# Optimization experiments

Hardware: AMD Instinct MI355X
Metric: run time of the kernel (lower is better)

Reference implementation:

```python
import math
import jax, jax.numpy as jnp
import numpy as np

N, L, C, H, E = 50000, 3, 64, 4, 800000
D = C // H


def setup_inputs() -> dict:
    key = jax.random.key(0)
    ks = jax.random.split(key, 10)
    s = 1.0 / math.sqrt(C)
    return {
        "history": jax.random.normal(ks[0], (N, L, C), dtype=jnp.float32),
        "edge_index": jax.random.randint(ks[1], (2, E), 0, N, dtype=jnp.int32),
        "Wq": jax.random.normal(ks[2], (C, C), dtype=jnp.float32) * s,
        "bq": jnp.zeros((C,), dtype=jnp.float32),
        "Wk": jax.random.normal(ks[3], (C, C), dtype=jnp.float32) * s,
        "bk": jnp.zeros((C,), dtype=jnp.float32),
        "Wv": jax.random.normal(ks[4], (C, C), dtype=jnp.float32) * s,
        "bv": jnp.zeros((C,), dtype=jnp.float32),
        "Wo": jax.random.normal(ks[5], (C, C), dtype=jnp.float32) * s,
        "bo": jnp.zeros((C,), dtype=jnp.float32),
    }


def reference(history, edge_index, Wq, bq, Wk, bk, Wv, bv, Wo, bo):
    row, col = edge_index[0], edge_index[1]
    current = history[:, -1]                                   # [N, C]
    # torch Linear: y = x @ W.T + b
    q = (current @ Wq.T + bq).reshape(N, H, D)                  # [N, H, D]
    k = (history @ Wk.T + bk).reshape(N, L, H, D)               # [N, L, H, D]
    v = (history @ Wv.T + bv).reshape(N, L, H, D)

    q_dst = q[col][:, None]                                     # [E, 1, H, D]
    k_src = k[row]                                              # [E, L, H, D]
    scores = (q_dst * k_src).sum(-1) / math.sqrt(D)             # [E, L, H]
    token_w = jax.nn.softmax(scores, axis=1)                    # layer attention
    edge_msg = (token_w[..., None] * v[row]).sum(axis=1)        # [E, H, D]

    # edge_softmax over incoming edges of each destination node (per head)
    edge_scores = scores.max(axis=1)                            # [E, H]
    seg_max = jax.ops.segment_max(edge_scores, col, num_segments=N)
    seg_max = jnp.where(jnp.isfinite(seg_max), seg_max, 0.0)
    e = jnp.exp(edge_scores - seg_max[col])                     # [E, H]
    denom = jax.ops.segment_sum(e, col, num_segments=N)         # [N, H]
    edge_w = e / denom[col]                                     # [E, H]

    out = jnp.zeros((N, H, D), dtype=current.dtype)
    out = out.at[col].add(edge_msg * edge_w[..., None])          # scatter-add
    out = out.reshape(N, C)
    return out @ Wo.T + bo + current
```

## Files before the change

kernel.cpp:

```cpp
#include <hip/hip_runtime.h>

#define DEV __device__ __forceinline__

constexpr int L = 3;
constexpr int C = 64;
constexpr int H = 4;
constexpr int CAP = 64;

typedef unsigned short ushort8v __attribute__((ext_vector_type(8)));
typedef unsigned short ushort4v __attribute__((ext_vector_type(4)));
typedef short short8v __attribute__((ext_vector_type(8)));
typedef float f32x4 __attribute__((ext_vector_type(4)));

DEV float4 ld4g(const float* p) { return *reinterpret_cast<const float4*>(p); }
DEV void st4g(float* p, float4 v) { *reinterpret_cast<float4*>(p) = v; }
DEV float b2f(unsigned short u) {
    union { float f; unsigned int i; } x; x.i = ((unsigned int)u) << 16; return x.f;
}
DEV unsigned short f2b(float f) {
    unsigned int u = __float_as_uint(f);
    return (unsigned short)((u + 0x7FFFu + ((u >> 16) & 1u)) >> 16);
}
DEV float dot8(float4 a, float4 b, ushort8v k) {
    return a.x*b2f(k[0]) + a.y*b2f(k[1]) + a.z*b2f(k[2]) + a.w*b2f(k[3])
         + b.x*b2f(k[4]) + b.y*b2f(k[5]) + b.z*b2f(k[6]) + b.w*b2f(k[7]);
}
DEV void acc8(float4& A, float4& B, float w, ushort8v v) {
    A.x = fmaf(w, b2f(v[0]), A.x); A.y = fmaf(w, b2f(v[1]), A.y);
    A.z = fmaf(w, b2f(v[2]), A.z); A.w = fmaf(w, b2f(v[3]), A.w);
    B.x = fmaf(w, b2f(v[4]), B.x); B.y = fmaf(w, b2f(v[5]), B.y);
    B.z = fmaf(w, b2f(v[6]), B.z); B.w = fmaf(w, b2f(v[7]), B.w);
}

__global__ __launch_bounds__(256) void qkv_kernel(
    const float* __restrict__ history,
    const float* __restrict__ Wk, const float* __restrict__ bk,
    const float* __restrict__ Wv, const float* __restrict__ bv,
    const float* __restrict__ Wq, const float* __restrict__ bq,
    unsigned short* __restrict__ kvout, float* __restrict__ qout,
    const int* __restrict__ ei, int* __restrict__ counts, int* __restrict__ srcs,
    int N, int E, int nkvBlocks)
{
    __shared__ __align__(16) unsigned short WL[2][4096];
    __shared__ __align__(16) unsigned short ST[4][2048];

    {
        int gid = blockIdx.x * 256 + threadIdx.x;
        if (gid < E) {
            int c = ei[E + gid];
            int r = atomicAdd(&counts[c], 1);
            if (r < CAP) srcs[c * CAP + r] = ei[gid];
        }
    }

    const bool isKV = (int)blockIdx.x < nkvBlocks;
    const int nqBlocks = (N + 63) / 64;
    if (!isKV && (int)blockIdx.x >= nkvBlocks + nqBlocks) return;
    const int rowBase = (isKV ? blockIdx.x : (blockIdx.x - nkvBlocks)) * 64;
    const int totalRows = isKV ? N * L : N;
    const int tid = threadIdx.x;

    {
        const float* W1 = isKV ? Wk : Wq;
        const int col = tid >> 2;
        const int kc = (tid & 3) << 4;
        #pragma unroll
        for (int g = 0; g < 2; ++g) {
            int k0 = kc + g * 8;
            float4 wa = ld4g(&W1[col * 64 + k0]);
            float4 wb = ld4g(&W1[col * 64 + k0 + 4]);
            ushort8v t;
            t[0] = f2b(wa.x); t[1] = f2b(wa.y); t[2] = f2b(wa.z); t[3] = f2b(wa.w);
            t[4] = f2b(wb.x); t[5] = f2b(wb.y); t[6] = f2b(wb.z); t[7] = f2b(wb.w);
            *(ushort8v*)&WL[0][(k0 >> 3) * 512 + col * 8] = t;
        }
        if (isKV) {
            #pragma unroll
            for (int g = 0; g < 2; ++g) {
                int k0 = kc + g * 8;
                float4 wa = ld4g(&Wv[col * 64 + k0]);
                float4 wb = ld4g(&Wv[col * 64 + k0 + 4]);
                ushort8v t;
                t[0] = f2b(wa.x); t[1] = f2b(wa.y); t[2] = f2b(wa.z); t[3] = f2b(wa.w);
                t[4] = f2b(wb.x); t[5] = f2b(wb.y); t[6] = f2b(wb.z); t[7] = f2b(wb.w);
                *(ushort8v*)&WL[1][(k0 >> 3) * 512 + col * 8] = t;
            }
        }
    }
    __syncthreads();

    const int lane = tid & 63;
    const int wid = tid >> 6;
    const int rbase = rowBase + wid * 16;
    const int kg = lane >> 4;
    const int kbase = kg << 3;
    const int bcol = lane & 15;

    const int arow = min(rbase + (lane & 15), totalRows - 1);
    const size_t srcRow = isKV ? (size_t)arow : ((size_t)arow * L + (L - 1));
    const float* xp = &history[srcRow * C];
    float4 xa = ld4g(xp + kbase), xb = ld4g(xp + kbase + 4);
    float4 xc = ld4g(xp + 32 + kbase), xd = ld4g(xp + 32 + kbase + 4);
    short8v a0, a1;
    a0[0] = (short)f2b(xa.x); a0[1] = (short)f2b(xa.y);
    a0[2] = (short)f2b(xa.z); a0[3] = (short)f2b(xa.w);
    a0[4] = (short)f2b(xb.x); a0[5] = (short)f2b(xb.y);
    a0[6] = (short)f2b(xb.z); a0[7] = (short)f2b(xb.w);
    a1[0] = (short)f2b(xc.x); a1[1] = (short)f2b(xc.y);
    a1[2] = (short)f2b(xc.z); a1[3] = (short)f2b(xc.w);
    a1[4] = (short)f2b(xd.x); a1[5] = (short)f2b(xd.y);
    a1[6] = (short)f2b(xd.z); a1[7] = (short)f2b(xd.w);

    const f32x4 zero = {0.f, 0.f, 0.f, 0.f};

    if (isKV) {
        f32x4 aK[4] = {zero, zero, zero, zero};
        f32x4 aV[4] = {zero, zero, zero, zero};
        #pragma unroll
        for (int ct = 0; ct < 4; ++ct) {
            int col = ct * 16 + bcol;
            short8v bk0 = *(const short8v*)&WL[0][(kg) * 512 + col * 8];
            short8v bk1 = *(const short8v*)&WL[0][(4 + kg) * 512 + col * 8];
            short8v bv0 = *(const short8v*)&WL[1][(kg) * 512 + col * 8];
            short8v bv1 = *(const short8v*)&WL[1][(4 + kg) * 512 + col * 8];
            aK[ct] = __builtin_amdgcn_mfma_f32_16x16x32_bf16(a0, bk0, aK[ct], 0, 0, 0);
            aK[ct] = __builtin_amdgcn_mfma_f32_16x16x32_bf16(a1, bk1, aK[ct], 0, 0, 0);
            aV[ct] = __builtin_amdgcn_mfma_f32_16x16x32_bf16(a0, bv0, aV[ct], 0, 0, 0);
            aV[ct] = __builtin_amdgcn_mfma_f32_16x16x32_bf16(a1, bv1, aV[ct], 0, 0, 0);
        }
        unsigned short* st = &ST[wid][0];
        #pragma unroll
        for (int ct = 0; ct < 4; ++ct) {
            int col = ct * 16 + bcol;
            float biasK = bk[col];
            float biasV = bv[col];
            #pragma unroll
            for (int i = 0; i < 4; ++i) {
                int r = kg * 4 + i;
                int ck = col, cv = 64 + col;
                int pk = r * 128 + ((((ck >> 3) ^ r) & 15) << 3) + (ck & 7);
                int pv = r * 128 + ((((cv >> 3) ^ r) & 15) << 3) + (cv & 7);
                st[pk] = f2b(aK[ct][i] + biasK);
                st[pv] = f2b(aV[ct][i] + biasV);
            }
        }
        asm volatile("s_waitcnt lgkmcnt(0)" ::: "memory");
        unsigned short* base = kvout + (size_t)rbase * 128;
        #pragma unroll
        for (int i = 0; i < 4; ++i) {
            int chunk = i * 64 + lane;
            int r = chunk >> 4;
            int cc = chunk & 15;
            if (rbase + r < totalRows) {
                ushort8v vls = *(const ushort8v*)&st[(r * 16 + ((cc ^ r) & 15)) * 8];
                *(ushort8v*)(base + chunk * 8) = vls;
            }
        }
    } else {
        f32x4 aQ[4] = {zero, zero, zero, zero};
        #pragma unroll
        for (int ct = 0; ct < 4; ++ct) {
            int col = ct * 16 + bcol;
            short8v bq0 = *(const short8v*)&WL[0][(kg) * 512 + col * 8];
            short8v bq1 = *(const short8v*)&WL[0][(4 + kg) * 512 + col * 8];
            aQ[ct] = __builtin_amdgcn_mfma_f32_16x16x32_bf16(a0, bq0, aQ[ct], 0, 0, 0);
            aQ[ct] = __builtin_amdgcn_mfma_f32_16x16x32_bf16(a1, bq1, aQ[ct], 0, 0, 0);
        }
        float* stf = (float*)&ST[wid][0];
        #pragma unroll
        for (int ct = 0; ct < 4; ++ct) {
            int col = ct * 16 + bcol;
            float bias = bq[col];
            #pragma unroll
            for (int i = 0; i < 4; ++i) {
                int r = kg * 4 + i;
                int p = r * 64 + ((((col >> 2) ^ r) & 15) << 2) + (col & 3);
                stf[p] = (aQ[ct][i] + bias) * 0.25f;
            }
        }
        asm volatile("s_waitcnt lgkmcnt(0)" ::: "memory");
        float* baseq = qout + (size_t)rbase * 64;
        #pragma unroll
        for (int i = 0; i < 4; ++i) {
            int chunk = i * 64 + lane;
            int r = chunk >> 4;
            int cc = chunk & 15;
            if (rbase + r < totalRows) {
                float4 vq = *(const float4*)&stf[(r * 16 + ((cc ^ r) & 15)) * 4];
                *(float4*)(baseq + chunk * 4) = vq;
            }
        }
    }
}

__global__ __launch_bounds__(256) void gather_kernel(
    const int* __restrict__ srcs, const int* __restrict__ counts,
    const float* __restrict__ q, const unsigned short* __restrict__ kv,
    const float* __restrict__ history,
    const float* __restrict__ Wo, const float* __restrict__ bo,
    float* __restrict__ out, int N)
{
    __shared__ __align__(16) unsigned short WoS[4096];
    __shared__ float boS[64];
    __shared__ float sc4[4][64];

    const int tid = threadIdx.x;
    #pragma unroll
    for (int j = 0; j < 16; ++j) {
        int idx = tid + (j << 8);
        int c = idx >> 6, i = idx & 63;
        int phys = (c << 6) | ((((i >> 2) ^ c) & 15) << 2) | (i & 3);
        WoS[phys] = f2b(Wo[idx]);
    }
    if (tid < 64) boS[tid] = bo[tid];
    __syncthreads();

    const int n = blockIdx.x * 4 + (tid >> 6);
    if (n >= N) return;
    const int lane = tid & 63;
    const int wid = tid >> 6;
    float* sc = &sc4[wid][0];

    const int sub = lane >> 3;
    const int ld = lane & 7;
    const int c0 = ld << 3;
    const int wrow = lane << 6;

    const int start = n * CAP;
    const int cnt = min(counts[n], CAP);

    const float xv = history[((size_t)n * L + (L - 1)) * C + lane];
    const float4 qa = ld4g(&q[(size_t)n * C + c0]);
    const float4 qb = ld4g(&q[(size_t)n * C + c0 + 4]);
    float4 ma = make_float4(0.f, 0.f, 0.f, 0.f);
    float4 mb = make_float4(0.f, 0.f, 0.f, 0.f);
    float dsum = 0.f;

    for (int i = sub; i < cnt; i += 8) {
        const int src = srcs[start + i];
        const unsigned short* kb = kv + (size_t)src * (L * 2 * C) + c0;
        ushort8v k0 = *(const ushort8v*)(kb);
        ushort8v k1 = *(const ushort8v*)(kb + 2 * C);
        ushort8v k2 = *(const ushort8v*)(kb + 4 * C);

        float s0 = dot8(qa, qb, k0);
        float s1 = dot8(qa, qb, k1);
        float s2 = dot8(qa, qb, k2);
        s0 += __shfl_xor(s0, 1);
        s1 += __shfl_xor(s1, 1);
        s2 += __shfl_xor(s2, 1);

        float e0 = __expf(s0), e1 = __expf(s1), e2 = __expf(s2);
        float ee = fmaxf(fmaxf(e0, e1), e2);
        float scl = ee / (e0 + e1 + e2);
        float w0 = e0 * scl, w1 = e1 * scl, w2 = e2 * scl;

        ushort8v v0 = *(const ushort8v*)(kb + C);
        ushort8v v1 = *(const ushort8v*)(kb + 3 * C);
        ushort8v v2 = *(const ushort8v*)(kb + 5 * C);
        acc8(ma, mb, w0, v0);
        acc8(ma, mb, w1, v1);
        acc8(ma, mb, w2, v2);
        dsum += ee;
    }

    #pragma unroll
    for (int m = 8; m <= 32; m <<= 1) {
        ma.x += __shfl_xor(ma.x, m); ma.y += __shfl_xor(ma.y, m);
        ma.z += __shfl_xor(ma.z, m); ma.w += __shfl_xor(ma.w, m);
        mb.x += __shfl_xor(mb.x, m); mb.y += __shfl_xor(mb.y, m);
        mb.z += __shfl_xor(mb.z, m); mb.w += __shfl_xor(mb.w, m);
        dsum += __shfl_xor(dsum, m);
    }

    if (sub == 0) {
        float inv = dsum > 0.f ? 1.f / dsum : 0.f;
        float4 oa, ob;
        oa.x = ma.x * inv; oa.y = ma.y * inv; oa.z = ma.z * inv; oa.w = ma.w * inv;
        ob.x = mb.x * inv; ob.y = mb.y * inv; ob.z = mb.z * inv; ob.w = mb.w * inv;
        *(float4*)&sc[c0] = oa;
        *(float4*)&sc[c0 + 4] = ob;
    }
    asm volatile("s_waitcnt lgkmcnt(0)" ::: "memory");
    float oc = boS[lane] + xv;
    #pragma unroll
    for (int j = 0; j < 16; ++j) {
        float4 aj = *(const float4*)&sc[j << 2];
        ushort4v w = *(const ushort4v*)&WoS[wrow | (((j ^ lane) & 15) << 2)];
        oc += aj.x * b2f(w[0]) + aj.y * b2f(w[1])
            + aj.z * b2f(w[2]) + aj.w * b2f(w[3]);
    }
    out[(size_t)n * C + lane] = oc;
}

extern "C" void kernel_launch(void* const* d_in, const int* in_sizes, int n_in,
                              void* d_out, int out_size, void* d_ws, size_t ws_size,
                              hipStream_t stream)
{
    const float* history = (const float*)d_in[0];
    const int*   ei      = (const int*)d_in[1];
    const float* Wq = (const float*)d_in[2];
    const float* bq = (const float*)d_in[3];
    const float* Wk = (const float*)d_in[4];
    const float* bk = (const float*)d_in[5];
    const float* Wv = (const float*)d_in[6];
    const float* bv = (const float*)d_in[7];
    const float* Wo = (const float*)d_in[8];
    const float* bo = (const float*)d_in[9];
    const int N = in_sizes[0] / (L * C);
    const int E = in_sizes[1] / 2;

    float* qbuf = (float*)d_ws;
    unsigned short* kvbuf = (unsigned short*)(qbuf + (size_t)N * C);
    int* counts = (int*)(kvbuf + (size_t)N * L * 2 * C);
    int* srcs   = counts + N;

    hipMemsetAsync(counts, 0, (size_t)N * sizeof(int), stream);

    const int nkv = (N * L + 63) / 64;
    const int nq  = (N + 63) / 64;
    const int eb  = (E + 255) / 256;
    int qkvBlocks = nkv + nq;
    if (qkvBlocks < eb) qkvBlocks = eb;
    qkv_kernel<<<qkvBlocks, 256, 0, stream>>>(history, Wk, bk, Wv, bv, Wq, bq,
                                              kvbuf, qbuf, ei, counts, srcs,
                                              N, E, nkv);

    gather_kernel<<<(N + 3) / 4, 256, 0, stream>>>(srcs, counts, qbuf, kvbuf,
                                                   history, Wo, bo,
                                                   (float*)d_out, N);
}
```

Before: 153.4 us.

## Precompute bf16 weights once, store q and source indices in 16-bit

Adds a single-block prep kernel that converts Wk, Wv, Wq (pre-scaled by 1/sqrt(D)) and Wo to bf16 in their LDS-ready layouts, so each qkv and gather block copies them with vector loads instead of converting fp32 per block. The q buffer becomes bf16 and the CSR source indices become 16-bit unsigned shorts, which halves the gather traffic for both. The cost is an extra kernel launch and reduced precision on q. Storing node ids as unsigned short only holds while N is below 65536, which is true for N=50000.

```diff
diff --git a/kernel.cpp b/kernel.cpp
--- a/kernel.cpp
+++ b/kernel.cpp
@@ -13,7 +13,6 @@
 typedef float f32x4 __attribute__((ext_vector_type(4)));
 
 DEV float4 ld4g(const float* p) { return *reinterpret_cast<const float4*>(p); }
-DEV void st4g(float* p, float4 v) { *reinterpret_cast<float4*>(p) = v; }
 DEV float b2f(unsigned short u) {
     union { float f; unsigned int i; } x; x.i = ((unsigned int)u) << 16; return x.f;
 }
@@ -32,13 +31,33 @@
     B.z = fmaf(w, b2f(v[6]), B.z); B.w = fmaf(w, b2f(v[7]), B.w);
 }
 
+__global__ __launch_bounds__(256) void prep_kernel(
+    const float* __restrict__ Wk, const float* __restrict__ Wv,
+    const float* __restrict__ Wq, const float* __restrict__ Wo,
+    unsigned short* __restrict__ Wf)
+{
+    const int tid = threadIdx.x;
+    #pragma unroll
+    for (int j = 0; j < 16; ++j) {
+        int idx = tid + (j << 8);
+        int c = idx >> 6, k = idx & 63;
+        int fp = (k >> 3) * 512 + c * 8 + (k & 7);
+        Wf[fp]            = f2b(Wk[idx]);
+        Wf[4096 + fp]     = f2b(Wv[idx]);
+        Wf[8192 + fp]     = f2b(Wq[idx] * 0.25f);
+        int gp = (c << 6) | ((((k >> 2) ^ c) & 15) << 2) | (k & 3);
+        Wf[12288 + gp]    = f2b(Wo[idx]);
+    }
+}
+
 __global__ __launch_bounds__(256) void qkv_kernel(
     const float* __restrict__ history,
-    const float* __restrict__ Wk, const float* __restrict__ bk,
-    const float* __restrict__ Wv, const float* __restrict__ bv,
-    const float* __restrict__ Wq, const float* __restrict__ bq,
-    unsigned short* __restrict__ kvout, float* __restrict__ qout,
-    const int* __restrict__ ei, int* __restrict__ counts, int* __restrict__ srcs,
+    const unsigned short* __restrict__ Wf,
+    const float* __restrict__ bk, const float* __restrict__ bv,
+    const float* __restrict__ bq,
+    unsigned short* __restrict__ kvout, unsigned short* __restrict__ qout,
+    const int* __restrict__ ei, int* __restrict__ counts,
+    unsigned short* __restrict__ srcs,
     int N, int E, int nkvBlocks)
 {
     __shared__ __align__(16) unsigned short WL[2][4096];
@@ -49,7 +68,7 @@
         if (gid < E) {
             int c = ei[E + gid];
             int r = atomicAdd(&counts[c], 1);
-            if (r < CAP) srcs[c * CAP + r] = ei[gid];
+            if (r < CAP) srcs[c * CAP + r] = (unsigned short)ei[gid];
         }
     }
 
@@ -61,30 +80,15 @@
     const int tid = threadIdx.x;
 
     {
-        const float* W1 = isKV ? Wk : Wq;
-        const int col = tid >> 2;
-        const int kc = (tid & 3) << 4;
-        #pragma unroll
-        for (int g = 0; g < 2; ++g) {
-            int k0 = kc + g * 8;
-            float4 wa = ld4g(&W1[col * 64 + k0]);
-            float4 wb = ld4g(&W1[col * 64 + k0 + 4]);
-            ushort8v t;
-            t[0] = f2b(wa.x); t[1] = f2b(wa.y); t[2] = f2b(wa.z); t[3] = f2b(wa.w);
-            t[4] = f2b(wb.x); t[5] = f2b(wb.y); t[6] = f2b(wb.z); t[7] = f2b(wb.w);
-            *(ushort8v*)&WL[0][(k0 >> 3) * 512 + col * 8] = t;
-        }
+        int o = tid << 4;
         if (isKV) {
-            #pragma unroll
-            for (int g = 0; g < 2; ++g) {
-                int k0 = kc + g * 8;
-                float4 wa = ld4g(&Wv[col * 64 + k0]);
-                float4 wb = ld4g(&Wv[col * 64 + k0 + 4]);
-                ushort8v t;
-                t[0] = f2b(wa.x); t[1] = f2b(wa.y); t[2] = f2b(wa.z); t[3] = f2b(wa.w);
-                t[4] = f2b(wb.x); t[5] = f2b(wb.y); t[6] = f2b(wb.z); t[7] = f2b(wb.w);
-                *(ushort8v*)&WL[1][(k0 >> 3) * 512 + col * 8] = t;
-            }
+            *(ushort8v*)&WL[0][o]     = *(const ushort8v*)&Wf[o];
+            *(ushort8v*)&WL[0][o + 8] = *(const ushort8v*)&Wf[o + 8];
+            *(ushort8v*)&WL[1][o]     = *(const ushort8v*)&Wf[4096 + o];
+            *(ushort8v*)&WL[1][o + 8] = *(const ushort8v*)&Wf[4096 + o + 8];
+        } else {
+            *(ushort8v*)&WL[0][o]     = *(const ushort8v*)&Wf[8192 + o];
+            *(ushort8v*)&WL[0][o + 8] = *(const ushort8v*)&Wf[8192 + o + 8];
         }
     }
     __syncthreads();
@@ -166,38 +170,38 @@
             aQ[ct] = __builtin_amdgcn_mfma_f32_16x16x32_bf16(a0, bq0, aQ[ct], 0, 0, 0);
             aQ[ct] = __builtin_amdgcn_mfma_f32_16x16x32_bf16(a1, bq1, aQ[ct], 0, 0, 0);
         }
-        float* stf = (float*)&ST[wid][0];
+        unsigned short* st = &ST[wid][0];
         #pragma unroll
         for (int ct = 0; ct < 4; ++ct) {
             int col = ct * 16 + bcol;
-            float bias = bq[col];
+            float bias = bq[col] * 0.25f;
             #pragma unroll
             for (int i = 0; i < 4; ++i) {
                 int r = kg * 4 + i;
-                int p = r * 64 + ((((col >> 2) ^ r) & 15) << 2) + (col & 3);
-                stf[p] = (aQ[ct][i] + bias) * 0.25f;
+                int p = r * 64 + ((((col >> 3) ^ r) & 7) << 3) + (col & 7);
+                st[p] = f2b(aQ[ct][i] + bias);
             }
         }
         asm volatile("s_waitcnt lgkmcnt(0)" ::: "memory");
-        float* baseq = qout + (size_t)rbase * 64;
-        #pragma unroll
-        for (int i = 0; i < 4; ++i) {
+        unsigned short* baseq = qout + (size_t)rbase * 64;
+        #pragma unroll
+        for (int i = 0; i < 2; ++i) {
             int chunk = i * 64 + lane;
-            int r = chunk >> 4;
-            int cc = chunk & 15;
+            int r = chunk >> 3;
+            int cc = chunk & 7;
             if (rbase + r < totalRows) {
-                float4 vq = *(const float4*)&stf[(r * 16 + ((cc ^ r) & 15)) * 4];
-                *(float4*)(baseq + chunk * 4) = vq;
+                ushort8v vq = *(const ushort8v*)&st[(r * 8 + ((cc ^ r) & 7)) * 8];
+                *(ushort8v*)(baseq + chunk * 8) = vq;
             }
         }
     }
 }
 
 __global__ __launch_bounds__(256) void gather_kernel(
-    const int* __restrict__ srcs, const int* __restrict__ counts,
-    const float* __restrict__ q, const unsigned short* __restrict__ kv,
+    const unsigned short* __restrict__ srcs, const int* __restrict__ counts,
+    const unsigned short* __restrict__ q, const unsigned short* __restrict__ kv,
     const float* __restrict__ history,
-    const float* __restrict__ Wo, const float* __restrict__ bo,
+    const unsigned short* __restrict__ Wf, const float* __restrict__ bo,
     float* __restrict__ out, int N)
 {
     __shared__ __align__(16) unsigned short WoS[4096];
@@ -205,12 +209,10 @@
     __shared__ float sc4[4][64];
 
     const int tid = threadIdx.x;
-    #pragma unroll
-    for (int j = 0; j < 16; ++j) {
-        int idx = tid + (j << 8);
-        int c = idx >> 6, i = idx & 63;
-        int phys = (c << 6) | ((((i >> 2) ^ c) & 15) << 2) | (i & 3);
-        WoS[phys] = f2b(Wo[idx]);
+    {
+        int o = tid << 4;
+        *(ushort8v*)&WoS[o]     = *(const ushort8v*)&Wf[12288 + o];
+        *(ushort8v*)&WoS[o + 8] = *(const ushort8v*)&Wf[12288 + o + 8];
     }
     if (tid < 64) boS[tid] = bo[tid];
     __syncthreads();
@@ -230,8 +232,10 @@
     const int cnt = min(counts[n], CAP);
 
     const float xv = history[((size_t)n * L + (L - 1)) * C + lane];
-    const float4 qa = ld4g(&q[(size_t)n * C + c0]);
-    const float4 qb = ld4g(&q[(size_t)n * C + c0 + 4]);
+    ushort8v q8 = *(const ushort8v*)&q[(size_t)n * C + c0];
+    float4 qa, qb;
+    qa.x = b2f(q8[0]); qa.y = b2f(q8[1]); qa.z = b2f(q8[2]); qa.w = b2f(q8[3]);
+    qb.x = b2f(q8[4]); qb.y = b2f(q8[5]); qb.z = b2f(q8[6]); qb.w = b2f(q8[7]);
     float4 ma = make_float4(0.f, 0.f, 0.f, 0.f);
     float4 mb = make_float4(0.f, 0.f, 0.f, 0.f);
     float dsum = 0.f;
@@ -310,23 +314,26 @@
     const int N = in_sizes[0] / (L * C);
     const int E = in_sizes[1] / 2;
 
-    float* qbuf = (float*)d_ws;
-    unsigned short* kvbuf = (unsigned short*)(qbuf + (size_t)N * C);
+    unsigned short* Wf    = (unsigned short*)d_ws;
+    unsigned short* qbuf  = Wf + 4 * 4096;
+    unsigned short* kvbuf = qbuf + (size_t)N * C;
     int* counts = (int*)(kvbuf + (size_t)N * L * 2 * C);
-    int* srcs   = counts + N;
+    unsigned short* srcs  = (unsigned short*)(counts + N);
 
     hipMemsetAsync(counts, 0, (size_t)N * sizeof(int), stream);
+
+    prep_kernel<<<1, 256, 0, stream>>>(Wk, Wv, Wq, Wo, Wf);
 
     const int nkv = (N * L + 63) / 64;
     const int nq  = (N + 63) / 64;
     const int eb  = (E + 255) / 256;
     int qkvBlocks = nkv + nq;
     if (qkvBlocks < eb) qkvBlocks = eb;
-    qkv_kernel<<<qkvBlocks, 256, 0, stream>>>(history, Wk, bk, Wv, bv, Wq, bq,
+    qkv_kernel<<<qkvBlocks, 256, 0, stream>>>(history, Wf, bk, bv, bq,
                                               kvbuf, qbuf, ei, counts, srcs,
                                               N, E, nkv);
 
     gather_kernel<<<(N + 3) / 4, 256, 0, stream>>>(srcs, counts, qbuf, kvbuf,
-                                                   history, Wo, bo,
+                                                   history, Wf, bo,
                                                    (float*)d_out, N);
 }
```

Result: faster. 150.0 us (-2.2%).
